# Optimization experiments

Hardware: AMD Instinct MI355X
Metric: run time of the kernel (lower is better)

Reference implementation:

```python
import jax, jax.numpy as jnp
import numpy as np

HEADS = 20          # SDXL 1280-dim blocks use 20 heads (head_dim=64)
GROUND_SCALE = 1.0  # self.scale in the module


def _mha(q, k, v):
    # q: [B,S,C], k/v: [B,L,C] -> out [B,S,C]; diffusers get_attention_scores math
    B, S, C = q.shape
    d = C // HEADS
    qh = q.reshape(B, S, HEADS, d)
    kh = k.reshape(B, k.shape[1], HEADS, d)
    vh = v.reshape(B, v.shape[1], HEADS, d)
    scores = jnp.einsum('bqhd,bkhd->bhqk', qh, kh) * (d ** -0.5)
    probs = jax.nn.softmax(scores, axis=-1)
    out = jnp.einsum('bhqk,bkhd->bqhd', probs, vh)
    return out.reshape(B, S, C)


def setup_inputs() -> dict:
    key = jax.random.key(0)
    ks = jax.random.split(key, 13)
    B, S, C = 4, 4096, 1280      # batch, latent tokens (64x64), hidden_size
    L, Dc = 77, 2048             # text context len, cross_attention_dim
    Dt = 768                     # text grounding dim
    Ntext, Nimg = 10, 40         # num_object*num_tokens_{text,image}
    s = 0.02
    return {
        'hidden_states': jax.random.normal(ks[0], (B, S, C), jnp.float32),
        'encoder_hidden_states': jax.random.normal(ks[1], (B, L, Dc), jnp.float32),
        'text_box_grounding_embeds': jax.random.normal(ks[2], (B, Ntext, Dt), jnp.float32),
        'image_box_grounding_embeds': jax.random.normal(ks[3], (B, Nimg, Dc), jnp.float32),
        'Wq': jax.random.normal(ks[4], (C, C), jnp.float32) * s,
        'Wk': jax.random.normal(ks[5], (Dc, C), jnp.float32) * s,
        'Wv': jax.random.normal(ks[6], (Dc, C), jnp.float32) * s,
        'Wk_text': jax.random.normal(ks[7], (Dt, C), jnp.float32) * s,
        'Wv_text': jax.random.normal(ks[8], (Dt, C), jnp.float32) * s,
        'Wk_image': jax.random.normal(ks[9], (Dc, C), jnp.float32) * s,
        'Wv_image': jax.random.normal(ks[10], (Dc, C), jnp.float32) * s,
        'Wo': jax.random.normal(ks[11], (C, C), jnp.float32) * s,
        'bo': jnp.zeros((C,), jnp.float32),
    }


def reference(hidden_states, encoder_hidden_states, text_box_grounding_embeds,
              image_box_grounding_embeds, Wq, Wk, Wv, Wk_text, Wv_text,
              Wk_image, Wv_image, Wo, bo):
    residual = hidden_states
    # projections
    q = hidden_states @ Wq                       # [B,S,C]
    k = encoder_hidden_states @ Wk               # [B,L,C]
    v = encoder_hidden_states @ Wv
    # text-grounding KV appended to the text context KV
    k_text = text_box_grounding_embeds @ Wk_text # [B,Ntext,C]
    v_text = text_box_grounding_embeds @ Wv_text
    k = jnp.concatenate([k, k_text], axis=1)
    v = jnp.concatenate([v, v_text], axis=1)
    hs = _mha(q, k, v)
    # stage-2 image-grounding branch: separate attention, residual blend
    k_img = image_box_grounding_embeds @ Wk_image  # [B,Nimg,C]
    v_img = image_box_grounding_embeds @ Wv_image
    hs_img = _mha(q, k_img, v_img)
    hs = hs + GROUND_SCALE * hs_img
    # output projection (to_out[0]); dropout (to_out[1]) is identity at eval
    hs = hs @ Wo + bo
    # residual_connection=True, rescale_output_factor=1.0
    return hs + residual
```

## Files before the change

kernel.cpp:

```cpp
#include <hip/hip_runtime.h>

typedef unsigned short u16;
typedef __attribute__((ext_vector_type(4)))  float  f32x4;
typedef __attribute__((ext_vector_type(8)))  short  s16x8;
typedef __attribute__((ext_vector_type(8)))  unsigned short u16x8;
typedef __attribute__((ext_vector_type(4)))  unsigned short u16x4;
typedef __attribute__((ext_vector_type(4)))  float  f4;

#define AS1(p) ((const __attribute__((address_space(1))) void*)(p))
#define AS3(p) ((__attribute__((address_space(3))) void*)(p))

__device__ __forceinline__ float bf2f(u16 u) {
    unsigned v = ((unsigned)u) << 16;
    return __builtin_bit_cast(float, v);
}
__device__ __forceinline__ u16 f2bf(float f) {
    unsigned u = __builtin_bit_cast(unsigned, f);
    unsigned r = u + 0x7FFFu + ((u >> 16) & 1u);
    return (u16)(r >> 16);
}

struct CastJobs { const float* in[4]; u16* out[4]; long b[3]; };
__global__ void cast4_kernel(CastJobs J, long total4) {
    long i = (long)blockIdx.x * blockDim.x + threadIdx.x;
    if (i >= total4) return;
    int j = (i >= J.b[0]) + (i >= J.b[1]) + (i >= J.b[2]);
    long k = i - (j ? J.b[j - 1] : 0);
    f4 v = ((const f4*)J.in[j])[k];
    u16x4 o;
    o[0] = f2bf(v.x); o[1] = f2bf(v.y); o[2] = f2bf(v.z); o[3] = f2bf(v.w);
    ((u16x4*)J.out[j])[k] = o;
}

struct TJobs { const float* in[8]; u16* out[8]; int K[8]; };
__global__ void transpose8_kernel(TJobs J) {
    const int N = 1280;
    const int j = blockIdx.z;
    const int K = J.K[j];
    const int kb = blockIdx.y * 32;
    if (kb >= K) return;
    const float* in = J.in[j];
    u16* out = J.out[j];
    __shared__ float tile[32][33];
    int nb = blockIdx.x * 32;
    int tx = threadIdx.x, ty = threadIdx.y;
#pragma unroll
    for (int r = 0; r < 32; r += 8)
        tile[ty + r][tx] = in[(size_t)(kb + ty + r) * N + nb + tx];
    __syncthreads();
#pragma unroll
    for (int r = 0; r < 32; r += 8)
        out[(size_t)(nb + ty + r) * K + kb + tx] = f2bf(tile[tx][ty + r]);
}

#define SB __builtin_amdgcn_sched_barrier(0)
#define GATE0 do { asm volatile("s_waitcnt vmcnt(0)" ::: "memory"); SB; } while (0)

template <int EPI>
__global__ __launch_bounds__(256, 2) void gemm_8p(
    const u16* __restrict__ A, const u16* __restrict__ Bt, void* __restrict__ outp,
    const float* __restrict__ bias, const u16* __restrict__ resid)
{
    const int K = 1280, N = 1280;
    __shared__ u16 lsA[2][128 * 64];
    __shared__ u16 lsB[2][160 * 64];

    const int bid = blockIdx.x;
    const int swz = (bid & 7) * 128 + (bid >> 3);
    const int m0 = (swz >> 3) * 128;
    const int n0 = (swz & 7) * 160;

    const int t = threadIdx.x;
    const int lane = t & 63, wid = t >> 6;
    const int wm = wid >> 1, wn = wid & 1;
    const int fr = lane & 15, hi = lane >> 4;
    const int fr7 = fr & 7;

    const int srow = t >> 3;
    const int sslot = (t & 7) ^ (srow & 7);
    const u16* gA = A  + (size_t)(m0 + srow) * K + sslot * 8;
    const u16* gB = Bt + (size_t)(n0 + srow) * K + sslot * 8;
    const size_t cK = (size_t)32 * K;

#define STGA(BUF, CC, KO) __builtin_amdgcn_global_load_lds(AS1(gA + (CC) * cK + (KO)), \
        AS3((char*)lsA + (BUF) * 16384 + (CC) * 4096 + t * 16), 16, 0, 0)
#define STGB(BUF, CC, KO) __builtin_amdgcn_global_load_lds(AS1(gB + (CC) * cK + (KO)), \
        AS3((char*)lsB + (BUF) * 20480 + (CC) * 4096 + t * 16), 16, 0, 0)

#define STG9(BUF, KO) do { \
    STGB(BUF, 0, KO); STGB(BUF, 1, KO); STGB(BUF, 2, KO); STGB(BUF, 3, KO); STGB(BUF, 4, KO); \
    STGA(BUF, 0, KO); STGA(BUF, 1, KO); STGA(BUF, 2, KO); STGA(BUF, 3, KO); \
} while (0)

    const char* lA0 = (const char*)lsA + (size_t)(wm * 64 + fr) * 128 + (((0 + hi) ^ fr7) << 4);
    const char* lA1 = (const char*)lsA + (size_t)(wm * 64 + fr) * 128 + (((4 + hi) ^ fr7) << 4);
    const char* lB0 = (const char*)lsB + (size_t)(wn * 80 + fr) * 128 + (((0 + hi) ^ fr7) << 4);
    const char* lB1 = (const char*)lsB + (size_t)(wn * 80 + fr) * 128 + (((4 + hi) ^ fr7) << 4);

    f32x4 acc[4][5];
#pragma unroll
    for (int i = 0; i < 4; i++)
#pragma unroll
        for (int j = 0; j < 5; j++)
            acc[i][j] = (f32x4){0.f, 0.f, 0.f, 0.f};

    s16x8 af[4], bfv[5];

#define DSRD2(BUF, KS) do { \
    _Pragma("unroll") for (int mi = 0; mi < 4; mi++) \
        af[mi] = *(const s16x8*)(((KS) ? lA1 : lA0) + (BUF) * 16384 + mi * 2048); \
    _Pragma("unroll") for (int nf = 0; nf < 5; nf++) \
        bfv[nf] = *(const s16x8*)(((KS) ? lB1 : lB0) + (BUF) * 20480 + nf * 2048); \
} while (0)

#define MM2 do { \
    _Pragma("unroll") for (int mi = 0; mi < 4; mi++) \
        _Pragma("unroll") for (int nf = 0; nf < 5; nf++) \
            acc[mi][nf] = __builtin_amdgcn_mfma_f32_16x16x32_bf16( \
                af[mi], bfv[nf], acc[mi][nf], 0, 0, 0); \
} while (0)

#define PHA(BUF, DOSTG, KO) do { \
    DSRD2(BUF, 0); \
    if (DOSTG) STG9((BUF) ^ 1, KO); \
    SB; \
    __builtin_amdgcn_s_barrier(); \
    SB; \
    asm volatile("s_waitcnt lgkmcnt(0)" ::: "memory"); \
    SB; \
    __builtin_amdgcn_s_setprio(1); \
    MM2; \
    __builtin_amdgcn_s_setprio(0); \
    SB; \
    __builtin_amdgcn_s_barrier(); \
    SB; \
} while (0)

#define PHB(BUF, DOGATE) do { \
    DSRD2(BUF, 1); \
    SB; \
    __builtin_amdgcn_s_barrier(); \
    SB; \
    asm volatile("s_waitcnt lgkmcnt(0)" ::: "memory"); \
    SB; \
    __builtin_amdgcn_s_setprio(1); \
    MM2; \
    __builtin_amdgcn_s_setprio(0); \
    SB; \
    if (DOGATE) { GATE0; } \
    __builtin_amdgcn_s_barrier(); \
    SB; \
} while (0)

    STG9(0, 0);
    GATE0;
    __builtin_amdgcn_s_barrier();
    SB;

    for (int i = 0; i < 9; i++) {
        const size_t k1 = (size_t)(2 * i + 1) * 64, k2 = k1 + 64;
        PHA(0, 1, k1); PHB(0, 1);
        PHA(1, 1, k2); PHB(1, 1);
    }
    PHA(0, 1, (size_t)19 * 64); PHB(0, 1);
    PHA(1, 0, 0);               PHB(1, 0);

#pragma unroll
    for (int mf = 0; mf < 4; mf++) {
#pragma unroll
        for (int nf = 0; nf < 5; nf++) {
#pragma unroll
            for (int j = 0; j < 4; j++) {
                int row = m0 + wm * 64 + mf * 16 + hi * 4 + j;
                int col = n0 + wn * 80 + nf * 16 + fr;
                float v = acc[mf][nf][j];
                if constexpr (EPI == 0) {
                    ((u16*)outp)[(size_t)row * N + col] = f2bf(v);
                } else {
                    ((float*)outp)[(size_t)row * N + col] =
                        v + bias[col] + bf2f(resid[(size_t)row * N + col]);
                }
            }
        }
    }
#undef STGA
#undef STGB
#undef STG9
#undef DSRD2
#undef MM2
#undef PHA
#undef PHB
}

struct KVJobs { const u16* A[6]; const u16* Bt[6]; float* out[6]; int M[6]; int K[6]; int gx[6]; };
__global__ __launch_bounds__(256) void gemm_kv(KVJobs J) {
    const int j = blockIdx.z;
    if ((int)blockIdx.x >= J.gx[j]) return;
    const u16* A  = J.A[j];
    const u16* Bt = J.Bt[j];
    float* outp   = J.out[j];
    const int M = J.M[j], K = J.K[j], N = 1280;

    __shared__ u16 lsA[2][128 * 32];
    __shared__ u16 lsB[2][128 * 32];

    const int m0 = blockIdx.x * 128, n0 = blockIdx.y * 128;
    const int t = threadIdx.x;
    const int lane = t & 63;
    const int wid = t >> 6;
    const int wr = wid >> 1, wc = wid & 1;
    const int fr = lane & 15;
    const int fq = lane >> 4;
    const int fk = fq * 8;

    f32x4 acc[4][4];
#pragma unroll
    for (int i = 0; i < 4; i++)
#pragma unroll
        for (int jj = 0; jj < 4; jj++)
            acc[i][jj] = (f32x4){0.f, 0.f, 0.f, 0.f};

    const int arow = t >> 2;
    const int acol = (t & 3) * 8;
    const u16* gA = A  + (size_t)(m0 + arow) * K + acol;
    const u16* gB = Bt + (size_t)(n0 + arow) * K + acol;

#define STAGE(buf, k0)                                                                                   \
    do {                                                                                                 \
        __builtin_amdgcn_global_load_lds(AS1(gA + (k0)),                  AS3(&lsA[buf][t * 8]),        16, 0, 0); \
        __builtin_amdgcn_global_load_lds(AS1(gA + (size_t)64 * K + (k0)), AS3(&lsA[buf][2048 + t * 8]), 16, 0, 0); \
        __builtin_amdgcn_global_load_lds(AS1(gB + (k0)),                  AS3(&lsB[buf][t * 8]),        16, 0, 0); \
        __builtin_amdgcn_global_load_lds(AS1(gB + (size_t)64 * K + (k0)), AS3(&lsB[buf][2048 + t * 8]), 16, 0, 0); \
    } while (0)

    STAGE(0, 0);
    __syncthreads();

    int cur = 0;
    for (int k0 = 0; k0 < K; k0 += 32) {
        if (k0 + 32 < K) STAGE(cur ^ 1, k0 + 32);

        s16x8 af[4], bfr[4];
#pragma unroll
        for (int i = 0; i < 4; i++) {
            af[i]  = *(const s16x8*)&lsA[cur][(wr * 64 + i * 16 + fr) * 32 + fk];
            bfr[i] = *(const s16x8*)&lsB[cur][(wc * 64 + i * 16 + fr) * 32 + fk];
        }
#pragma unroll
        for (int mi = 0; mi < 4; mi++)
#pragma unroll
            for (int ni = 0; ni < 4; ni++)
                acc[mi][ni] = __builtin_amdgcn_mfma_f32_16x16x32_bf16(af[mi], bfr[ni], acc[mi][ni], 0, 0, 0);

        __syncthreads();
        cur ^= 1;
    }
#undef STAGE

#pragma unroll
    for (int mi = 0; mi < 4; mi++) {
#pragma unroll
        for (int ni = 0; ni < 4; ni++) {
#pragma unroll
            for (int jj = 0; jj < 4; jj++) {
                int row = m0 + wr * 64 + mi * 16 + fq * 4 + jj;
                int col = n0 + wc * 64 + ni * 16 + fr;
                if (row < M)
                    outp[(size_t)row * N + col] = acc[mi][ni][jj];
            }
        }
    }
}

__global__ void gather_kv(
    const float* __restrict__ k77, const float* __restrict__ v77,
    const float* __restrict__ ktx, const float* __restrict__ vtx,
    const float* __restrict__ kim, const float* __restrict__ vim,
    u16* __restrict__ Kimg, u16* __restrict__ Vimg)
{
    const int bh = blockIdx.x;
    const int b = bh / 20, h = bh - b * 20;
    const int t = threadIdx.x;
    char* Kd = (char*)(Kimg + (size_t)bh * 8192);
    char* Vd = (char*)(Vimg + (size_t)bh * 8192);

#pragma unroll
    for (int i = 0; i < 4; i++) {
        int ch = t + i * 256;
        int r = ch >> 3, cs = ch & 7;
        u16x8 ov = (u16x8){0,0,0,0,0,0,0,0};
        if (r < 127) {
            const float* src = r < 77 ? k77 + ((size_t)b * 77 + r) * 1280
                            : r < 87  ? ktx + ((size_t)b * 10 + (r - 77)) * 1280
                                      : kim + ((size_t)b * 40 + (r - 87)) * 1280;
            const f4* s4 = (const f4*)(src + h * 64 + cs * 8);
            f4 a = s4[0], c = s4[1];
            ov[0]=f2bf(a.x*0.125f); ov[1]=f2bf(a.y*0.125f); ov[2]=f2bf(a.z*0.125f); ov[3]=f2bf(a.w*0.125f);
            ov[4]=f2bf(c.x*0.125f); ov[5]=f2bf(c.y*0.125f); ov[6]=f2bf(c.z*0.125f); ov[7]=f2bf(c.w*0.125f);
        }
        *(u16x8*)(Kd + ((r * 128 + cs * 16) ^ ((r & 7) << 4))) = ov;
    }

#pragma unroll
    for (int i = 0; i < 4; i++) {
        int ch = t + i * 256;
        int d = ch & 63, ks = ch >> 6;
        u16x8 ov;
#pragma unroll
        for (int j = 0; j < 8; j++) {
            int key = ks * 8 + j;
            float val = key < 77  ? v77[((size_t)b * 77 + key) * 1280 + h * 64 + d]
                      : key < 87  ? vtx[((size_t)b * 10 + key - 77) * 1280 + h * 64 + d]
                      : key < 127 ? vim[((size_t)b * 40 + key - 87) * 1280 + h * 64 + d]
                                  : 0.f;
            ov[j] = f2bf(val);
        }
        *(u16x8*)(Vd + ((d * 256 + ks * 16) ^ ((d & 7) << 4))) = ov;
    }
}

__global__ __launch_bounds__(256) void attn_mfma(
    const u16* __restrict__ q, const u16* __restrict__ Kimg,
    const u16* __restrict__ Vimg, u16* __restrict__ out)
{
    __shared__ char sm[49152];
    char* Qb = sm;
    char* Kb = sm + 16384;
    char* Vb = sm + 32768;

    const int t = threadIdx.x;
    const int lane = t & 63, wid = t >> 6;
    const int lo = lane & 15, hi = lane >> 4;
    const int s0 = blockIdx.x * 128;
    const int bh = blockIdx.y;
    const int b = bh / 20, h = bh - b * 20;
    const size_t rs0 = (size_t)b * 4096 + s0;

    const u16* gk = Kimg + (size_t)bh * 8192;
    const u16* gv = Vimg + (size_t)bh * 8192;
#pragma unroll
    for (int i = 0; i < 4; i++) {
        int ch = t + i * 256;
        __builtin_amdgcn_global_load_lds(AS1(gk + (size_t)ch * 8), AS3(Kb + ch * 16), 16, 0, 0);
        __builtin_amdgcn_global_load_lds(AS1(gv + (size_t)ch * 8), AS3(Vb + ch * 16), 16, 0, 0);
    }
#pragma unroll
    for (int i = 0; i < 4; i++) {
        int ch = t + i * 256;
        int r = ch >> 3, cs = ch & 7;
        u16x8 v = *(const u16x8*)(q + (rs0 + r) * 1280 + h * 64 + cs * 8);
        *(u16x8*)(Qb + ((r * 128 + cs * 16) ^ ((r & 7) << 4))) = v;
    }
    __syncthreads();

    const int m0r = wid * 32;
    s16x8 qf[2][2];
#pragma unroll
    for (int m = 0; m < 2; m++)
#pragma unroll
        for (int kf = 0; kf < 2; kf++) {
            int r = m0r + m * 16 + lo;
            qf[m][kf] = *(const s16x8*)(Qb + ((r * 128 + (kf * 4 + hi) * 16) ^ ((r & 7) << 4)));
        }
    f32x4 sc[2][8];
#pragma unroll
    for (int m = 0; m < 2; m++)
#pragma unroll
        for (int n = 0; n < 8; n++)
            sc[m][n] = (f32x4){0.f, 0.f, 0.f, 0.f};
#pragma unroll
    for (int kf = 0; kf < 2; kf++)
#pragma unroll
        for (int n = 0; n < 8; n++) {
            int r = n * 16 + lo;
            s16x8 kf8 = *(const s16x8*)(Kb + ((r * 128 + (kf * 4 + hi) * 16) ^ ((r & 7) << 4)));
#pragma unroll
            for (int m = 0; m < 2; m++)
                sc[m][n] = __builtin_amdgcn_mfma_f32_16x16x32_bf16(qf[m][kf], kf8, sc[m][n], 0, 0, 0);
        }
    __syncthreads();

    char* Pb = sm + wid * 8192;
#pragma unroll
    for (int m = 0; m < 2; m++) {
#pragma unroll
        for (int j = 0; j < 4; j++) {
            float e[8];
            float s1 = 0.f, s2 = 0.f;
#pragma unroll
            for (int n = 0; n < 8; n++) {
                int col = n * 16 + lo;
                float ev = __expf(sc[m][n][j]);
                e[n] = ev;
                if (col < 87) s1 += ev;
                else if (col < 127) s2 += ev;
            }
#pragma unroll
            for (int d = 1; d < 16; d <<= 1) {
                s1 += __shfl_xor(s1, d);
                s2 += __shfl_xor(s2, d);
            }
            float i1 = 1.f / s1, i2 = 1.f / s2;
            int row = m * 16 + hi * 4 + j;
#pragma unroll
            for (int n = 0; n < 8; n++) {
                int col = n * 16 + lo;
                float w = col < 87 ? i1 : (col < 127 ? i2 : 0.f);
                *(u16*)(Pb + ((row * 256 + col * 2) ^ ((row & 7) << 4))) = f2bf(e[n] * w);
            }
        }
    }
    __syncthreads();

    f32x4 o2[2][4];
#pragma unroll
    for (int m = 0; m < 2; m++)
#pragma unroll
        for (int n = 0; n < 4; n++)
            o2[m][n] = (f32x4){0.f, 0.f, 0.f, 0.f};
#pragma unroll
    for (int kk = 0; kk < 4; kk++) {
        s16x8 pa[2];
#pragma unroll
        for (int m = 0; m < 2; m++) {
            int row = m * 16 + lo;
            pa[m] = *(const s16x8*)(Pb + ((row * 256 + (kk * 4 + hi) * 16) ^ ((row & 7) << 4)));
        }
#pragma unroll
        for (int n = 0; n < 4; n++) {
            int dr = n * 16 + lo;
            s16x8 vf = *(const s16x8*)(Vb + ((dr * 256 + (kk * 4 + hi) * 16) ^ ((dr & 7) << 4)));
#pragma unroll
            for (int m = 0; m < 2; m++)
                o2[m][n] = __builtin_amdgcn_mfma_f32_16x16x32_bf16(pa[m], vf, o2[m][n], 0, 0, 0);
        }
    }

#pragma unroll
    for (int m = 0; m < 2; m++)
#pragma unroll
        for (int n = 0; n < 4; n++)
#pragma unroll
            for (int j = 0; j < 4; j++) {
                size_t row = rs0 + m0r + m * 16 + hi * 4 + j;
                out[row * 1280 + h * 64 + n * 16 + lo] = f2bf(o2[m][n][j]);
            }
}

extern "C" void kernel_launch(void* const* d_in, const int* in_sizes, int n_in,
                              void* d_out, int out_size, void* d_ws, size_t ws_size,
                              hipStream_t stream)
{
    const float* hs  = (const float*)d_in[0];
    const float* ehs = (const float*)d_in[1];
    const float* tbg = (const float*)d_in[2];
    const float* ibg = (const float*)d_in[3];
    const float* Wq  = (const float*)d_in[4];
    const float* Wk  = (const float*)d_in[5];
    const float* Wv  = (const float*)d_in[6];
    const float* Wkt = (const float*)d_in[7];
    const float* Wvt = (const float*)d_in[8];
    const float* Wki = (const float*)d_in[9];
    const float* Wvi = (const float*)d_in[10];
    const float* Wo  = (const float*)d_in[11];
    const float* bo  = (const float*)d_in[12];
    float* out = (float*)d_out;

    const int B = 4, S = 4096, C = 1280, L = 77, Nt = 10, Ni = 40, Dc = 2048, Dt = 768;
    const int M = B * S;

    char* p = (char*)d_ws;
    auto alloc = [&](size_t bytes) -> void* {
        void* r = (void*)p;
        p += (bytes + 255) & ~(size_t)255;
        return r;
    };
    u16* hs_b  = (u16*)alloc((size_t)M * C * 2);
    u16* q_b   = (u16*)alloc((size_t)M * C * 2);
    u16* at_b  = (u16*)alloc((size_t)M * C * 2);
    u16* WqT   = (u16*)alloc((size_t)C * C * 2);
    u16* WoT   = (u16*)alloc((size_t)C * C * 2);
    u16* WkT   = (u16*)alloc((size_t)C * Dc * 2);
    u16* WvT   = (u16*)alloc((size_t)C * Dc * 2);
    u16* WkiT  = (u16*)alloc((size_t)C * Dc * 2);
    u16* WviT  = (u16*)alloc((size_t)C * Dc * 2);
    u16* WktT  = (u16*)alloc((size_t)C * Dt * 2);
    u16* WvtT  = (u16*)alloc((size_t)C * Dt * 2);
    u16* ehs_b = (u16*)alloc((size_t)384 * Dc * 2);
    u16* tbg_b = (u16*)alloc((size_t)128 * Dt * 2);
    u16* ibg_b = (u16*)alloc((size_t)256 * Dc * 2);
    float* k77 = (float*)alloc((size_t)B * L  * C * 4);
    float* v77 = (float*)alloc((size_t)B * L  * C * 4);
    float* ktx = (float*)alloc((size_t)B * Nt * C * 4);
    float* vtx = (float*)alloc((size_t)B * Nt * C * 4);
    float* kim = (float*)alloc((size_t)B * Ni * C * 4);
    float* vim = (float*)alloc((size_t)B * Ni * C * 4);
    u16* Kimg  = (u16*)alloc((size_t)80 * 8192 * 2);
    u16* Vimg  = (u16*)alloc((size_t)80 * 8192 * 2);

    CastJobs cj;
    cj.in[0] = hs;  cj.out[0] = hs_b;
    cj.in[1] = ehs; cj.out[1] = ehs_b;
    cj.in[2] = tbg; cj.out[2] = tbg_b;
    cj.in[3] = ibg; cj.out[3] = ibg_b;
    long c0 = (long)M * C / 4, c1 = (long)B * L * Dc / 4,
         c2 = (long)B * Nt * Dt / 4, c3 = (long)B * Ni * Dc / 4;
    cj.b[0] = c0; cj.b[1] = c0 + c1; cj.b[2] = c0 + c1 + c2;
    long total4 = c0 + c1 + c2 + c3;
    cast4_kernel<<<(int)((total4 + 255) / 256), 256, 0, stream>>>(cj, total4);

    TJobs tj;
    const float* wins[8] = {Wq, Wk, Wv, Wkt, Wvt, Wki, Wvi, Wo};
    u16* wouts[8]        = {WqT, WkT, WvT, WktT, WvtT, WkiT, WviT, WoT};
    int wks[8]           = {C, Dc, Dc, Dt, Dt, Dc, Dc, C};
    for (int i = 0; i < 8; i++) { tj.in[i] = wins[i]; tj.out[i] = wouts[i]; tj.K[i] = wks[i]; }
    transpose8_kernel<<<dim3(C / 32, Dc / 32, 8), dim3(32, 8), 0, stream>>>(tj);

    gemm_8p<0><<<1024, 256, 0, stream>>>(hs_b, WqT, q_b, nullptr, nullptr);

    KVJobs kj;
    const u16* kas[6]  = {ehs_b, ehs_b, tbg_b, tbg_b, ibg_b, ibg_b};
    const u16* kbs[6]  = {WkT, WvT, WktT, WvtT, WkiT, WviT};
    float* kos[6]      = {k77, v77, ktx, vtx, kim, vim};
    int kms[6]         = {B * L, B * L, B * Nt, B * Nt, B * Ni, B * Ni};
    int kks[6]         = {Dc, Dc, Dt, Dt, Dc, Dc};
    int kgx[6]         = {3, 3, 1, 1, 2, 2};
    for (int i = 0; i < 6; i++) {
        kj.A[i] = kas[i]; kj.Bt[i] = kbs[i]; kj.out[i] = kos[i];
        kj.M[i] = kms[i]; kj.K[i] = kks[i]; kj.gx[i] = kgx[i];
    }
    gemm_kv<<<dim3(3, C / 128, 6), 256, 0, stream>>>(kj);

    gather_kv<<<80, 256, 0, stream>>>(k77, v77, ktx, vtx, kim, vim, Kimg, Vimg);
    attn_mfma<<<dim3(S / 128, B * 20), 256, 0, stream>>>(q_b, Kimg, Vimg, at_b);

    gemm_8p<2><<<1024, 256, 0, stream>>>(at_b, WoT, out, bo, hs_b);
}
```

Measured before the change: 256.0 us.

## Restructure projection GEMM to 256x160 tiles with triple-buffered K=32 pipeline

Replaces the 128x160 double-buffered GEMM (K-step 64, 256 threads) with a 256x160 tile using 512 threads (8 waves) and a three-stage LDS ring of K=32 slices. A partial vmcnt wait keeps one stage of global->LDS loads in flight while computing. The aim is better latency hiding and more reuse of B per block. In exchange there are more barriers per K and a new swizzle and load layout that must be correct.

After: 301.5 us. +17.8%, slower.

```diff
diff --git a/kernel.cpp b/kernel.cpp
--- a/kernel.cpp
+++ b/kernel.cpp
@@ -54,48 +54,48 @@
 }
 
 #define SB __builtin_amdgcn_sched_barrier(0)
+#define GATE4 do { asm volatile("s_waitcnt vmcnt(4)" ::: "memory"); SB; } while (0)
 #define GATE0 do { asm volatile("s_waitcnt vmcnt(0)" ::: "memory"); SB; } while (0)
+#define NOGATE
 
 template <int EPI>
-__global__ __launch_bounds__(256, 2) void gemm_8p(
+__global__ __launch_bounds__(512, 4) void gemm_3b(
     const u16* __restrict__ A, const u16* __restrict__ Bt, void* __restrict__ outp,
     const float* __restrict__ bias, const u16* __restrict__ resid)
 {
     const int K = 1280, N = 1280;
-    __shared__ u16 lsA[2][128 * 64];
-    __shared__ u16 lsB[2][160 * 64];
+    __shared__ u16 lsA[3][256 * 32];
+    __shared__ u16 lsB[3][160 * 32];
 
     const int bid = blockIdx.x;
-    const int swz = (bid & 7) * 128 + (bid >> 3);
-    const int m0 = (swz >> 3) * 128;
+    const int swz = (bid & 7) * 64 + (bid >> 3);
+    const int m0 = (swz >> 3) * 256;
     const int n0 = (swz & 7) * 160;
 
     const int t = threadIdx.x;
     const int lane = t & 63, wid = t >> 6;
     const int wm = wid >> 1, wn = wid & 1;
     const int fr = lane & 15, hi = lane >> 4;
-    const int fr7 = fr & 7;
-
-    const int srow = t >> 3;
-    const int sslot = (t & 7) ^ (srow & 7);
-    const u16* gA = A  + (size_t)(m0 + srow) * K + sslot * 8;
-    const u16* gB = Bt + (size_t)(n0 + srow) * K + sslot * 8;
-    const size_t cK = (size_t)32 * K;
-
-#define STGA(BUF, CC, KO) __builtin_amdgcn_global_load_lds(AS1(gA + (CC) * cK + (KO)), \
-        AS3((char*)lsA + (BUF) * 16384 + (CC) * 4096 + t * 16), 16, 0, 0)
-#define STGB(BUF, CC, KO) __builtin_amdgcn_global_load_lds(AS1(gB + (CC) * cK + (KO)), \
-        AS3((char*)lsB + (BUF) * 20480 + (CC) * 4096 + t * 16), 16, 0, 0)
-
-#define STG9(BUF, KO) do { \
-    STGB(BUF, 0, KO); STGB(BUF, 1, KO); STGB(BUF, 2, KO); STGB(BUF, 3, KO); STGB(BUF, 4, KO); \
-    STGA(BUF, 0, KO); STGA(BUF, 1, KO); STGA(BUF, 2, KO); STGA(BUF, 3, KO); \
+
+    const int srow = t >> 2;
+    const int sslot = (t & 3) ^ ((t >> 2) & 3);
+    const u16* gA  = A  + (size_t)(m0 + srow) * K + sslot * 8;
+    const u16* gB  = Bt + (size_t)(n0 + srow) * K + sslot * 8;
+    const u16* gBp = Bt + (size_t)(n0 + 128 + ((t & 127) >> 2)) * K + sslot * 8;
+    const size_t cK = (size_t)128 * K;
+
+    char* lsAc = (char*)lsA;
+    char* lsBc = (char*)lsB;
+
+#define STG(BUF, KO) do { \
+    __builtin_amdgcn_global_load_lds(AS1(gA + (KO)),       AS3(lsAc + (BUF) * 16384 + t * 16),                 16, 0, 0); \
+    __builtin_amdgcn_global_load_lds(AS1(gA + cK + (KO)),  AS3(lsAc + (BUF) * 16384 + 8192 + t * 16),          16, 0, 0); \
+    __builtin_amdgcn_global_load_lds(AS1(gB + (KO)),       AS3(lsBc + (BUF) * 10240 + t * 16),                 16, 0, 0); \
+    __builtin_amdgcn_global_load_lds(AS1(gBp + (KO)),      AS3(lsBc + (BUF) * 10240 + 8192 + (t & 127) * 16),  16, 0, 0); \
 } while (0)
 
-    const char* lA0 = (const char*)lsA + (size_t)(wm * 64 + fr) * 128 + (((0 + hi) ^ fr7) << 4);
-    const char* lA1 = (const char*)lsA + (size_t)(wm * 64 + fr) * 128 + (((4 + hi) ^ fr7) << 4);
-    const char* lB0 = (const char*)lsB + (size_t)(wn * 80 + fr) * 128 + (((0 + hi) ^ fr7) << 4);
-    const char* lB1 = (const char*)lsB + (size_t)(wn * 80 + fr) * 128 + (((4 + hi) ^ fr7) << 4);
+    const char* lA = lsAc + (size_t)(wm * 64 + fr) * 64 + ((hi ^ (fr & 3)) << 4);
+    const char* lB = lsBc + (size_t)(wn * 80 + fr) * 64 + ((hi ^ (fr & 3)) << 4);
 
     f32x4 acc[4][5];
 #pragma unroll
@@ -106,64 +106,52 @@
 
     s16x8 af[4], bfv[5];
 
-#define DSRD2(BUF, KS) do { \
+#define DSRD(BUF) do { \
     _Pragma("unroll") for (int mi = 0; mi < 4; mi++) \
-        af[mi] = *(const s16x8*)(((KS) ? lA1 : lA0) + (BUF) * 16384 + mi * 2048); \
+        af[mi] = *(const s16x8*)(lA + (BUF) * 16384 + mi * 1024); \
     _Pragma("unroll") for (int nf = 0; nf < 5; nf++) \
-        bfv[nf] = *(const s16x8*)(((KS) ? lB1 : lB0) + (BUF) * 20480 + nf * 2048); \
+        bfv[nf] = *(const s16x8*)(lB + (BUF) * 10240 + nf * 1024); \
 } while (0)
 
-#define MM2 do { \
+#define MM do { \
     _Pragma("unroll") for (int mi = 0; mi < 4; mi++) \
         _Pragma("unroll") for (int nf = 0; nf < 5; nf++) \
             acc[mi][nf] = __builtin_amdgcn_mfma_f32_16x16x32_bf16( \
                 af[mi], bfv[nf], acc[mi][nf], 0, 0, 0); \
 } while (0)
 
-#define PHA(BUF, DOSTG, KO) do { \
-    DSRD2(BUF, 0); \
-    if (DOSTG) STG9((BUF) ^ 1, KO); \
+#define PH(BUF, SBUF, DOSTG, KO, GT) do { \
+    DSRD(BUF); \
+    if (DOSTG) STG(SBUF, KO); \
     SB; \
     __builtin_amdgcn_s_barrier(); \
     SB; \
     asm volatile("s_waitcnt lgkmcnt(0)" ::: "memory"); \
     SB; \
     __builtin_amdgcn_s_setprio(1); \
-    MM2; \
+    MM; \
     __builtin_amdgcn_s_setprio(0); \
     SB; \
+    GT; \
     __builtin_amdgcn_s_barrier(); \
     SB; \
 } while (0)
 
-#define PHB(BUF, DOGATE) do { \
-    DSRD2(BUF, 1); \
-    SB; \
-    __builtin_amdgcn_s_barrier(); \
-    SB; \
-    asm volatile("s_waitcnt lgkmcnt(0)" ::: "memory"); \
-    SB; \
-    __builtin_amdgcn_s_setprio(1); \
-    MM2; \
-    __builtin_amdgcn_s_setprio(0); \
-    SB; \
-    if (DOGATE) { GATE0; } \
-    __builtin_amdgcn_s_barrier(); \
-    SB; \
-} while (0)
-
-    STG9(0, 0);
-    GATE0;
+    STG(0, 0); STG(1, 32);
+    GATE4;
     __builtin_amdgcn_s_barrier();
     SB;
 
-    for (int i = 0; i < 9; i++) {
-        const size_t k1 = (size_t)(2 * i + 1) * 64, k2 = k1 + 64;
-        PHA(0, 1, k1); PHB(0, 1);
-        PHA(1, 1, k2); PHB(1, 1);
-    }
-    PHA(0, 1, (size_t)19 * 64); PHB(0, 1);
-    PHA(1, 0, 0);               PHB(1, 0);
+    for (int i = 0; i < 12; i++) {
+        const int k2 = (3 * i + 2) * 32;
+        PH(0, 2, 1, k2,      GATE4);
+        PH(1, 0, 1, k2 + 32, GATE4);
+        PH(2, 1, 1, k2 + 64, GATE4);
+    }
+    PH(0, 2, 1, 38 * 32, GATE4);
+    PH(1, 0, 1, 39 * 32, GATE4);
+    PH(2, 0, 0, 0,       GATE0);
+    PH(0, 0, 0, 0,       NOGATE);
 
 #pragma unroll
     for (int mf = 0; mf < 4; mf++) {
@@ -183,13 +171,10 @@
             }
         }
     }
-#undef STGA
-#undef STGB
-#undef STG9
-#undef DSRD2
-#undef MM2
-#undef PHA
-#undef PHB
+#undef STG
+#undef DSRD
+#undef MM
+#undef PH
 }
 
 struct KVJobs { const u16* A[6]; const u16* Bt[6]; float* out[6]; int M[6]; int K[6]; int gx[6]; };
@@ -516,7 +501,7 @@
     for (int i = 0; i < 8; i++) { tj.in[i] = wins[i]; tj.out[i] = wouts[i]; tj.K[i] = wks[i]; }
     transpose8_kernel<<<dim3(C / 32, Dc / 32, 8), dim3(32, 8), 0, stream>>>(tj);
 
-    gemm_8p<0><<<1024, 256, 0, stream>>>(hs_b, WqT, q_b, nullptr, nullptr);
+    gemm_3b<0><<<512, 512, 0, stream>>>(hs_b, WqT, q_b, nullptr, nullptr);
 
     KVJobs kj;
     const u16* kas[6]  = {ehs_b, ehs_b, tbg_b, tbg_b, ibg_b, ibg_b};
@@ -534,5 +519,5 @@
     gather_kv<<<80, 256, 0, stream>>>(k77, v77, ktx, vtx, kim, vim, Kimg, Vimg);
     attn_mfma<<<dim3(S / 128, B * 20), 256, 0, stream>>>(q_b, Kimg, Vimg, at_b);
 
-    gemm_8p<2><<<1024, 256, 0, stream>>>(at_b, WoT, out, bo, hs_b);
-}
+    gemm_3b<2><<<512, 512, 0, stream>>>(at_b, WoT, out, bo, hs_b);
+}
```
